# Kernel tuning notes

Measured on AMD Instinct MI355X. Metric: run time of the kernel, lower is better.

The kernel has to match this reference:

```python
import jax, jax.numpy as jnp
import numpy as np

N, M, K, D = 65536, 131072, 8, 64
TAU = 0.3
EPS = 1e-6

def setup_inputs() -> dict:
    key = jax.random.key(0)
    ks = jax.random.split(key, 16)
    s = 0.05
    return {
        "f_pts": jax.random.normal(ks[0], (N, D), jnp.float32),
        "pts": jax.random.uniform(ks[1], (N, 3), jnp.float32) * 10.0,
        "z_latent": jax.random.normal(ks[2], (M, D), jnp.float32) * 0.1,
        "centers": jax.random.uniform(ks[3], (M, 3), jnp.float32) * 10.0,
        "cand_idx": jax.random.randint(ks[4], (N, K), 0, M),
        "sim_w1": jax.random.normal(ks[5], (2 * D + 3, 64), jnp.float32) * s,
        "sim_b1": jnp.zeros((64,), jnp.float32),
        "sim_w2": jax.random.normal(ks[6], (64, 1), jnp.float32) * s,
        "sim_b2": jnp.zeros((1,), jnp.float32),
        "gate_w1": jax.random.normal(ks[7], (2 * D, D), jnp.float32) * s,
        "gate_b1": jnp.zeros((D,), jnp.float32),
        "gate_w2": jax.random.normal(ks[8], (D, 1), jnp.float32) * s,
        "gate_b2": jnp.zeros((1,), jnp.float32),
        "W_ih": jax.random.normal(ks[9], (3 * D, D), jnp.float32) * s,
        "W_hh": jax.random.normal(ks[10], (3 * D, D), jnp.float32) * s,
        "b_ih": jnp.zeros((3 * D,), jnp.float32),
        "b_hh": jnp.zeros((3 * D,), jnp.float32),
    }

def _forward(f_pts, pts, z_latent, centers, sim_w1, sim_b1, sim_w2, sim_b2,
             gate_w1, gate_b1, gate_w2, gate_b2, W_ih, W_hh, b_ih, b_hh, cand_idx):
    n, k = cand_idx.shape
    m, d = z_latent.shape
    # --- gather voxel latents / centers for each (point, candidate) pair ---
    z_c = z_latent[cand_idx]                         # (N,K,D)
    delta = pts[:, None, :] - centers[cand_idx]      # (N,K,3)
    f_b = jnp.broadcast_to(f_pts[:, None, :], (n, k, d))
    # --- similarity MLP ---
    x = jnp.concatenate([f_b, z_c, delta], axis=-1)  # (N,K,2D+3)
    h = jax.nn.relu(x @ sim_w1 + sim_b1)
    sim = (h @ sim_w2 + sim_b2)[..., 0]              # (N,K)
    # --- low-temperature top-K routing weights over candidates ---
    w = jax.nn.softmax(sim / TAU, axis=-1)           # (N,K)
    # --- scatter weighted point features to voxels ---
    flat_idx = cand_idx.reshape(-1)                  # (N*K,)
    contrib = (w[..., None] * f_pts[:, None, :]).reshape(-1, d)
    msg = jax.ops.segment_sum(contrib, flat_idx, num_segments=m)     # (M,D)
    wsum = jax.ops.segment_sum(w.reshape(-1), flat_idx, num_segments=m)
    msg = msg / (wsum[:, None] + EPS)                # normalized voxel message
    # --- per-voxel gate ---
    g_in = jnp.concatenate([z_latent, msg], axis=-1)
    gate = jax.nn.sigmoid(jax.nn.relu(g_in @ gate_w1 + gate_b1) @ gate_w2 + gate_b2)  # (M,1)
    # --- GRUCell (torch layout: rows ordered r,z,n) ---
    gi = msg @ W_ih.T + b_ih
    gh = z_latent @ W_hh.T + b_hh
    i_r, i_z, i_n = jnp.split(gi, 3, axis=-1)
    h_r, h_z, h_n = jnp.split(gh, 3, axis=-1)
    r = jax.nn.sigmoid(i_r + h_r)
    zg = jax.nn.sigmoid(i_z + h_z)
    nn_ = jnp.tanh(i_n + r * h_n)
    h_new = (1.0 - zg) * nn_ + zg * z_latent
    # gated latent update
    return z_latent + gate * (h_new - z_latent)

def reference(f_pts, pts, z_latent, centers, cand_idx, sim_w1, sim_b1, sim_w2, sim_b2,
              gate_w1, gate_b1, gate_w2, gate_b2, W_ih, W_hh, b_ih, b_hh):
    return _forward(f_pts, pts, z_latent, centers, sim_w1, sim_b1, sim_w2, sim_b2,
                    gate_w1, gate_b1, gate_w2, gate_b2, W_ih, W_hh, b_ih, b_hh, cand_idx)
```

## Files before the change

kernel.cpp:

```cpp
#include <hip/hip_runtime.h>
#include <hip/hip_fp16.h>
#include <math.h>


typedef short bf16x8 __attribute__((ext_vector_type(8)));
typedef unsigned short u16x8 __attribute__((ext_vector_type(8)));
typedef float f32x4 __attribute__((ext_vector_type(4)));
#define MFMA __builtin_amdgcn_mfma_f32_16x16x32_bf16
#define CAP 32

__device__ __forceinline__ short f2bf(float f) {
  unsigned u = __float_as_uint(f);
  unsigned r = (u + 0x7FFFu + ((u >> 16) & 1u)) >> 16;
  return (short)r;
}

__device__ __forceinline__ float bf2f(unsigned short h) {
  return __uint_as_float(((unsigned)h) << 16);
}

__device__ __forceinline__ float sigm(float x) { return 1.0f / (1.0f + __expf(-x)); }

__global__ __launch_bounds__(256) void prep_kernel(
    const float* __restrict__ z, const float* __restrict__ f,
    const float* __restrict__ pts, const float* __restrict__ centers,
    const float* __restrict__ sim_w1, const float* __restrict__ sim_b1,
    const float* __restrict__ gate_w1, const float* __restrict__ W_ih,
    const float* __restrict__ W_hh,
    unsigned short* __restrict__ zbf, unsigned short* __restrict__ fbf,
    unsigned short* __restrict__ HBp, unsigned short* __restrict__ ZC,
    short* __restrict__ GF, short* __restrict__ WihF, short* __restrict__ WhhF,
    int* __restrict__ cursor, int M)
{
  long tid = (long)blockIdx.x * 256 + threadIdx.x;
  long nthr = (long)gridDim.x * 256;

  for (long i = tid; i < M; i += nthr) cursor[i] = 0;

  long nz = (long)M * 64;
  for (long i = tid * 8; i < nz; i += nthr * 8) {
    float4 a = *(const float4*)&z[i];
    float4 b4 = *(const float4*)&z[i + 4];
    u16x8 o;
    o[0] = (unsigned short)f2bf(a.x);  o[1] = (unsigned short)f2bf(a.y);
    o[2] = (unsigned short)f2bf(a.z);  o[3] = (unsigned short)f2bf(a.w);
    o[4] = (unsigned short)f2bf(b4.x); o[5] = (unsigned short)f2bf(b4.y);
    o[6] = (unsigned short)f2bf(b4.z); o[7] = (unsigned short)f2bf(b4.w);
    *(u16x8*)&zbf[i] = o;
  }

  if (blockIdx.x >= 1024 && blockIdx.x < 1040) {
    int fb = (blockIdx.x - 1024) * 4 + (threadIdx.x >> 6);
    int lane = threadIdx.x & 63, lr = lane & 15, lg = lane >> 4;
    bf16x8 o;
    if (fb < 16) {
      int ct = fb >> 2, kt = fb & 3;
#pragma unroll
      for (int e = 0; e < 8; ++e)
        o[e] = f2bf(gate_w1[(kt * 32 + lg * 8 + e) * 64 + ct * 16 + lr]);
      *(bf16x8*)&GF[fb * 512 + lane * 8] = o;
    } else if (fb < 40) {
      int q = fb - 16, g = q >> 3, ct = (q >> 1) & 3, k2 = q & 1;
      int row = g * 64 + ct * 16 + lr;
#pragma unroll
      for (int e = 0; e < 8; ++e)
        o[e] = f2bf(W_ih[row * 64 + k2 * 32 + lg * 8 + e]);
      *(bf16x8*)&WihF[q * 512 + lane * 8] = o;
    } else {
      int q = fb - 40, g = q >> 3, ct = (q >> 1) & 3, k2 = q & 1;
      int row = g * 64 + ct * 16 + lr;
#pragma unroll
      for (int e = 0; e < 8; ++e)
        o[e] = f2bf(W_hh[row * 64 + k2 * 32 + lg * 8 + e]);
      *(bf16x8*)&WhhF[q * 512 + lane * 8] = o;
    }
  }

  int g = blockIdx.x * 4 + (threadIdx.x >> 6);
  int lane = threadIdx.x & 63;
  int lr = lane & 15, lg = lane >> 4;

  if (g < 4096) {
    int n0 = g * 16;
    bf16x8 bw[12];
#pragma unroll
    for (int ct = 0; ct < 4; ++ct) {
#pragma unroll
      for (int kt = 0; kt < 2; ++kt) {
        bf16x8 bb;
#pragma unroll
        for (int e = 0; e < 8; ++e)
          bb[e] = f2bf(sim_w1[(kt * 32 + lg * 8 + e) * 64 + ct * 16 + lr]);
        bw[ct * 3 + kt] = bb;
      }
      bf16x8 bb = {0,0,0,0,0,0,0,0};
#pragma unroll
      for (int e = 0; e < 8; ++e) {
        int kk = lg * 8 + e;
        if (kk < 3) bb[e] = f2bf(sim_w1[(128 + kk) * 64 + ct * 16 + lr]);
      }
      bw[ct * 3 + 2] = bb;
    }

    bf16x8 a[3];
#pragma unroll
    for (int kt = 0; kt < 2; ++kt) {
      const float* src = &f[(long)(n0 + lr) * 64 + kt * 32 + lg * 8];
      float4 v0 = *(const float4*)src;
      float4 v1 = *(const float4*)(src + 4);
      bf16x8 t;
      t[0] = f2bf(v0.x); t[1] = f2bf(v0.y); t[2] = f2bf(v0.z); t[3] = f2bf(v0.w);
      t[4] = f2bf(v1.x); t[5] = f2bf(v1.y); t[6] = f2bf(v1.z); t[7] = f2bf(v1.w);
      a[kt] = t;
    }
    {
      bf16x8 t = {0,0,0,0,0,0,0,0};
      if (lg == 0) {
        t[0] = f2bf(pts[(n0 + lr) * 3 + 0]);
        t[1] = f2bf(pts[(n0 + lr) * 3 + 1]);
        t[2] = f2bf(pts[(n0 + lr) * 3 + 2]);
      }
      a[2] = t;
    }
    *(bf16x8*)&fbf[(long)(n0 + lr) * 64 + lg * 8] = a[0];
    *(bf16x8*)&fbf[(long)(n0 + lr) * 64 + 32 + lg * 8] = a[1];

    f32x4 acc[4] = {{0,0,0,0},{0,0,0,0},{0,0,0,0},{0,0,0,0}};
#pragma unroll
    for (int ct = 0; ct < 4; ++ct)
#pragma unroll
      for (int kt = 0; kt < 3; ++kt)
        acc[ct] = MFMA(a[kt], bw[ct * 3 + kt], acc[ct], 0, 0, 0);

#pragma unroll
    for (int ct = 0; ct < 4; ++ct) {
      float b1 = sim_b1[ct * 16 + lr];
#pragma unroll
      for (int e = 0; e < 4; ++e)
        HBp[(long)(n0 + lg * 4 + e) * 64 + ct * 16 + lr] =
            (unsigned short)f2bf(acc[ct][e] + b1);
    }
  } else if (g < 12288) {
    int r0 = (g - 4096) * 16;
    bf16x8 bw[12];
#pragma unroll
    for (int ct = 0; ct < 4; ++ct) {
#pragma unroll
      for (int kt = 0; kt < 2; ++kt) {
        bf16x8 bb;
#pragma unroll
        for (int e = 0; e < 8; ++e)
          bb[e] = f2bf(sim_w1[(64 + kt * 32 + lg * 8 + e) * 64 + ct * 16 + lr]);
        bw[ct * 3 + kt] = bb;
      }
      bf16x8 bb = {0,0,0,0,0,0,0,0};
#pragma unroll
      for (int e = 0; e < 8; ++e) {
        int kk = lg * 8 + e;
        if (kk < 3) bb[e] = f2bf(sim_w1[(128 + kk) * 64 + ct * 16 + lr]);
      }
      bw[ct * 3 + 2] = bb;
    }

    bf16x8 a[3];
#pragma unroll
    for (int kt = 0; kt < 2; ++kt) {
      const float* src = &z[(long)(r0 + lr) * 64 + kt * 32 + lg * 8];
      float4 v0 = *(const float4*)src;
      float4 v1 = *(const float4*)(src + 4);
      bf16x8 t;
      t[0] = f2bf(v0.x); t[1] = f2bf(v0.y); t[2] = f2bf(v0.z); t[3] = f2bf(v0.w);
      t[4] = f2bf(v1.x); t[5] = f2bf(v1.y); t[6] = f2bf(v1.z); t[7] = f2bf(v1.w);
      a[kt] = t;
    }
    {
      bf16x8 t = {0,0,0,0,0,0,0,0};
      if (lg == 0) {
        t[0] = f2bf(-centers[(r0 + lr) * 3 + 0]);
        t[1] = f2bf(-centers[(r0 + lr) * 3 + 1]);
        t[2] = f2bf(-centers[(r0 + lr) * 3 + 2]);
      }
      a[2] = t;
    }

    f32x4 acc[4] = {{0,0,0,0},{0,0,0,0},{0,0,0,0},{0,0,0,0}};
#pragma unroll
    for (int ct = 0; ct < 4; ++ct)
#pragma unroll
      for (int kt = 0; kt < 3; ++kt)
        acc[ct] = MFMA(a[kt], bw[ct * 3 + kt], acc[ct], 0, 0, 0);

#pragma unroll
    for (int ct = 0; ct < 4; ++ct)
#pragma unroll
      for (int e = 0; e < 4; ++e)
        ZC[(long)(r0 + lg * 4 + e) * 64 + ct * 16 + lr] =
            (unsigned short)f2bf(acc[ct][e]);
  }
}

__global__ __launch_bounds__(256) void pair_kernel(
    const unsigned short* __restrict__ HBp, const unsigned short* __restrict__ ZC,
    const int* __restrict__ cand_idx, const float* __restrict__ sim_w2,
    int* __restrict__ cursor, unsigned* __restrict__ rec)
{
  int n = (blockIdx.x * 256 + threadIdx.x) >> 6;
  int lane = threadIdx.x & 63;

  int ci = cand_idx[n * 8 + (lane & 7)];
  int c0 = __builtin_amdgcn_readlane(ci, 0);
  int c1 = __builtin_amdgcn_readlane(ci, 1);
  int c2 = __builtin_amdgcn_readlane(ci, 2);
  int c3 = __builtin_amdgcn_readlane(ci, 3);
  int c4 = __builtin_amdgcn_readlane(ci, 4);
  int c5 = __builtin_amdgcn_readlane(ci, 5);
  int c6 = __builtin_amdgcn_readlane(ci, 6);
  int c7 = __builtin_amdgcn_readlane(ci, 7);

  float hbv = bf2f(HBp[(long)n * 64 + lane]);
  float w2 = sim_w2[lane];
  float p0 = fmaxf(hbv + bf2f(ZC[(long)c0 * 64 + lane]), 0.f) * w2;
  float p1 = fmaxf(hbv + bf2f(ZC[(long)c1 * 64 + lane]), 0.f) * w2;
  float p2 = fmaxf(hbv + bf2f(ZC[(long)c2 * 64 + lane]), 0.f) * w2;
  float p3 = fmaxf(hbv + bf2f(ZC[(long)c3 * 64 + lane]), 0.f) * w2;
  float p4 = fmaxf(hbv + bf2f(ZC[(long)c4 * 64 + lane]), 0.f) * w2;
  float p5 = fmaxf(hbv + bf2f(ZC[(long)c5 * 64 + lane]), 0.f) * w2;
  float p6 = fmaxf(hbv + bf2f(ZC[(long)c6 * 64 + lane]), 0.f) * w2;
  float p7 = fmaxf(hbv + bf2f(ZC[(long)c7 * 64 + lane]), 0.f) * w2;

#pragma unroll
  for (int m = 1; m <= 32; m <<= 1) {
    p0 += __shfl_xor(p0, m, 64);
    p1 += __shfl_xor(p1, m, 64);
    p2 += __shfl_xor(p2, m, 64);
    p3 += __shfl_xor(p3, m, 64);
    p4 += __shfl_xor(p4, m, 64);
    p5 += __shfl_xor(p5, m, 64);
    p6 += __shfl_xor(p6, m, 64);
    p7 += __shfl_xor(p7, m, 64);
  }

  float mx = fmaxf(fmaxf(fmaxf(p0, p1), fmaxf(p2, p3)),
                   fmaxf(fmaxf(p4, p5), fmaxf(p6, p7)));
  float e0 = __expf((p0 - mx) * (1.0f / 0.3f));
  float e1 = __expf((p1 - mx) * (1.0f / 0.3f));
  float e2 = __expf((p2 - mx) * (1.0f / 0.3f));
  float e3 = __expf((p3 - mx) * (1.0f / 0.3f));
  float e4 = __expf((p4 - mx) * (1.0f / 0.3f));
  float e5 = __expf((p5 - mx) * (1.0f / 0.3f));
  float e6 = __expf((p6 - mx) * (1.0f / 0.3f));
  float e7 = __expf((p7 - mx) * (1.0f / 0.3f));
  float inv = 1.0f / (e0 + e1 + e2 + e3 + e4 + e5 + e6 + e7);

  if (lane < 8) {
    float wsel = lane == 0 ? e0 : lane == 1 ? e1 : lane == 2 ? e2 :
                 lane == 3 ? e3 : lane == 4 ? e4 : lane == 5 ? e5 :
                 lane == 6 ? e6 : e7;
    wsel *= inv;
    int slot = atomicAdd(&cursor[ci], 1);
    if (slot < CAP) {
      unsigned short wh = __half_as_ushort(__float2half(wsel));
      rec[(long)ci * CAP + slot] = ((unsigned)n << 16) | (unsigned)wh;
    }
  }
}

__global__ __launch_bounds__(256) void gather_kernel(
    const unsigned* __restrict__ rec, const int* __restrict__ cursor,
    const unsigned short* __restrict__ fbf, unsigned short* __restrict__ msg_bf,
    int mvox)
{
  int tid = blockIdx.x * 256 + threadIdx.x;
  int row = tid >> 2, seg = tid & 3;
  if (row >= mvox) return;

  int cnt = cursor[row];
  cnt = cnt < CAP ? cnt : CAP;
  const unsigned* rp = &rec[(long)row * CAP];

  float acc[16];
#pragma unroll
  for (int j = 0; j < 16; ++j) acc[j] = 0.f;
  float ws = 0.f;

  for (int i0 = 0; i0 < cnt; i0 += 4) {
    uint4 r4 = *(const uint4*)&rp[i0];
    unsigned rr0 = r4.x, rr1 = r4.y, rr2 = r4.z, rr3 = r4.w;
#pragma unroll
    for (int j = 0; j < 4; ++j) {
      unsigned r = j == 0 ? rr0 : j == 1 ? rr1 : j == 2 ? rr2 : rr3;
      if (i0 + j < cnt) {
        float w = __half2float(__ushort_as_half((unsigned short)(r & 0xffffu)));
        int nn = r >> 16;
        ws += w;
        const u16x8* fp = (const u16x8*)&fbf[(long)nn * 64 + seg * 16];
        u16x8 f0 = fp[0], f1 = fp[1];
#pragma unroll
        for (int k = 0; k < 8; ++k) {
          acc[k]     = fmaf(w, bf2f(f0[k]), acc[k]);
          acc[8 + k] = fmaf(w, bf2f(f1[k]), acc[8 + k]);
        }
      }
    }
  }
  float inv = 1.0f / (ws + 1e-6f);
  u16x8 o0, o1;
#pragma unroll
  for (int j = 0; j < 8; ++j) {
    o0[j] = (unsigned short)f2bf(acc[j] * inv);
    o1[j] = (unsigned short)f2bf(acc[8 + j] * inv);
  }
  *(u16x8*)&msg_bf[(long)row * 64 + seg * 16] = o0;
  *(u16x8*)&msg_bf[(long)row * 64 + seg * 16 + 8] = o1;
}

__global__ __launch_bounds__(512)
__attribute__((amdgpu_waves_per_eu(2)))
void stage2(
    const unsigned short* __restrict__ zbf,
    const short* __restrict__ GF, const short* __restrict__ WihF,
    const short* __restrict__ WhhF,
    const float* __restrict__ gate_b1, const float* __restrict__ gate_w2,
    const float* __restrict__ gate_b2,
    const float* __restrict__ b_ih, const float* __restrict__ b_hh,
    const unsigned short* __restrict__ msg_bf,
    float* __restrict__ out)
{
  __shared__ float gb1s[64], gw2s[64], bihs[192], bhhs[192];
  __shared__ float gb2s;

  int t = threadIdx.x;
  if (t < 64) { gb1s[t] = gate_b1[t]; gw2s[t] = gate_w2[t]; }
  if (t < 192) { bihs[t] = b_ih[t]; bhhs[t] = b_hh[t]; }
  if (t == 0) gb2s = gate_b2[0];
  __syncthreads();

  int wid = t >> 6, lane = t & 63;
  int lr = lane & 15, lg = lane >> 4;

  int rowbase = blockIdx.x * 128 + wid * 16;
  long abase = (long)(rowbase + lr) * 64;
  bf16x8 a0 = *(const bf16x8*)&zbf[abase + lg * 8];
  bf16x8 a1 = *(const bf16x8*)&zbf[abase + 32 + lg * 8];
  bf16x8 a2 = *(const bf16x8*)&msg_bf[abase + lg * 8];
  bf16x8 a3 = *(const bf16x8*)&msg_bf[abase + 32 + lg * 8];

  f32x4 usum = {0.f, 0.f, 0.f, 0.f};
#pragma unroll 1
  for (int ct = 0; ct < 4; ++ct) {
    f32x4 au = {0, 0, 0, 0};
    au = MFMA(a0, *(const bf16x8*)&GF[(ct * 4 + 0) * 512 + lane * 8], au, 0, 0, 0);
    au = MFMA(a1, *(const bf16x8*)&GF[(ct * 4 + 1) * 512 + lane * 8], au, 0, 0, 0);
    au = MFMA(a2, *(const bf16x8*)&GF[(ct * 4 + 2) * 512 + lane * 8], au, 0, 0, 0);
    au = MFMA(a3, *(const bf16x8*)&GF[(ct * 4 + 3) * 512 + lane * 8], au, 0, 0, 0);
    int c = ct * 16 + lr;
#pragma unroll
    for (int e = 0; e < 4; ++e)
      usum[e] += fmaxf(au[e] + gb1s[c], 0.0f) * gw2s[c];
  }
#pragma unroll
  for (int m = 1; m <= 8; m <<= 1)
#pragma unroll
    for (int e = 0; e < 4; ++e) {
      float v = usum[e];
      usum[e] = v + __shfl_xor(v, m, 64);
    }
  float gate[4];
#pragma unroll
  for (int e = 0; e < 4; ++e) gate[e] = sigm(usum[e] + gb2s);

#pragma unroll 1
  for (int ct = 0; ct < 4; ++ct) {
    f32x4 air = {0,0,0,0}, aiz = {0,0,0,0}, ain = {0,0,0,0};
    f32x4 ahr = {0,0,0,0}, ahz = {0,0,0,0}, ahn = {0,0,0,0};
#pragma unroll
    for (int k2 = 0; k2 < 2; ++k2) {
      bf16x8 amg = k2 ? a3 : a2;
      bf16x8 az_ = k2 ? a1 : a0;
      int base = ct * 2 + k2;
      air = MFMA(amg, *(const bf16x8*)&WihF[(      base) * 512 + lane * 8], air, 0, 0, 0);
      aiz = MFMA(amg, *(const bf16x8*)&WihF[( 8 +  base) * 512 + lane * 8], aiz, 0, 0, 0);
      ain = MFMA(amg, *(const bf16x8*)&WihF[(16 +  base) * 512 + lane * 8], ain, 0, 0, 0);
      ahr = MFMA(az_, *(const bf16x8*)&WhhF[(      base) * 512 + lane * 8], ahr, 0, 0, 0);
      ahz = MFMA(az_, *(const bf16x8*)&WhhF[( 8 +  base) * 512 + lane * 8], ahz, 0, 0, 0);
      ahn = MFMA(az_, *(const bf16x8*)&WhhF[(16 +  base) * 512 + lane * 8], ahn, 0, 0, 0);
    }
    int c = ct * 16 + lr;
#pragma unroll
    for (int e = 0; e < 4; ++e) {
      float zv = bf2f(zbf[(long)(rowbase + lg * 4 + e) * 64 + c]);
      float rr = sigm(air[e] + bihs[c] + ahr[e] + bhhs[c]);
      float zg = sigm(aiz[e] + bihs[64 + c] + ahz[e] + bhhs[64 + c]);
      float nn = tanhf(ain[e] + bihs[128 + c] + rr * (ahn[e] + bhhs[128 + c]));
      float hnew = (1.0f - zg) * nn + zg * zv;
      out[(long)(rowbase + lg * 4 + e) * 64 + c] = zv + gate[e] * (hnew - zv);
    }
  }
}

extern "C" void kernel_launch(void* const* d_in, const int* in_sizes, int n_in,
                              void* d_out, int out_size, void* d_ws, size_t ws_size,
                              hipStream_t stream) {
  const float* f_pts   = (const float*)d_in[0];
  const float* pts     = (const float*)d_in[1];
  const float* z_lat   = (const float*)d_in[2];
  const float* centers = (const float*)d_in[3];
  const int*   cand    = (const int*)d_in[4];
  const float* sim_w1  = (const float*)d_in[5];
  const float* sim_b1  = (const float*)d_in[6];
  const float* sim_w2  = (const float*)d_in[7];
  const float* gate_w1 = (const float*)d_in[9];
  const float* gate_b1 = (const float*)d_in[10];
  const float* gate_w2 = (const float*)d_in[11];
  const float* gate_b2 = (const float*)d_in[12];
  const float* W_ih    = (const float*)d_in[13];
  const float* W_hh    = (const float*)d_in[14];
  const float* b_ih    = (const float*)d_in[15];
  const float* b_hh    = (const float*)d_in[16];

  int N = in_sizes[0] / 64;
  int M = in_sizes[2] / 64;

  int* cursor = (int*)d_ws;
  unsigned* rec = (unsigned*)(cursor + M);
  unsigned short* msg_bf = (unsigned short*)rec;
  unsigned short* zbf = (unsigned short*)(rec + (size_t)M * CAP);
  unsigned short* fbf = zbf + (size_t)M * 64;
  unsigned short* HBp = fbf + (size_t)N * 64;
  unsigned short* ZC = HBp + (size_t)N * 64;
  short* GF = (short*)(ZC + (size_t)M * 64);
  short* WihF = GF + 16 * 512;
  short* WhhF = WihF + 24 * 512;

  prep_kernel<<<3072, 256, 0, stream>>>(z_lat, f_pts, pts, centers,
                                        sim_w1, sim_b1, gate_w1, W_ih, W_hh,
                                        zbf, fbf, HBp, ZC, GF, WihF, WhhF,
                                        cursor, M);

  pair_kernel<<<N / 4, 256, 0, stream>>>(HBp, ZC, cand, sim_w2, cursor, rec);

  gather_kernel<<<(M * 4) / 256, 256, 0, stream>>>(rec, cursor, fbf, msg_bf, M);

  stage2<<<M / 128, 512, 0, stream>>>(zbf, GF, WihF, WhhF,
                                      gate_b1, gate_w2, gate_b2, b_ih, b_hh,
                                      msg_bf, (float*)d_out);
}
```

Measured before the change: 119.3 us.

## Precompute weight fragments once, fuse z bf16 conversion, vectorize pair scoring

Adds a small prep0 kernel that converts all weight matrices to bf16 MFMA fragment layout once and zeroes the cursor array, so each prep wave loads ready fragments instead of reconverting sim_w1 from fp32. The separate z-to-bf16 loop is removed; the z fragments already loaded for the ZC projection are written out as zbf. The pair kernel is restructured so each lane handles one candidate and an 8-element channel slice with vector loads, shrinking the shuffle reductions and exp count. It adds one more kernel launch and relies on the new fragment buffers being laid out correctly in the workspace.

Result: faster. 102.4 us (-14.2%).

```diff
diff --git a/kernel.cpp b/kernel.cpp
--- a/kernel.cpp
+++ b/kernel.cpp
@@ -21,61 +21,76 @@
 
 __device__ __forceinline__ float sigm(float x) { return 1.0f / (1.0f + __expf(-x)); }
 
+__global__ __launch_bounds__(256) void prep0_kernel(
+    const float* __restrict__ sim_w1, const float* __restrict__ gate_w1,
+    const float* __restrict__ W_ih, const float* __restrict__ W_hh,
+    short* __restrict__ bfF, short* __restrict__ bfZC,
+    short* __restrict__ GF, short* __restrict__ WihF, short* __restrict__ WhhF,
+    int* __restrict__ cursor, int M)
+{
+  int tid = blockIdx.x * 256 + threadIdx.x;
+  int n4 = M >> 2;
+  int stride = gridDim.x * 256;
+  int4* cp = (int4*)cursor;
+  for (int j = tid; j < n4; j += stride) cp[j] = make_int4(0, 0, 0, 0);
+
+  int w = blockIdx.x * 4 + (threadIdx.x >> 6);
+  int lane = threadIdx.x & 63, lr = lane & 15, lg = lane >> 4;
+  bf16x8 o;
+
+  if (w < 12) {
+    int ct = w / 3, kt = w % 3;
+#pragma unroll
+    for (int e = 0; e < 8; ++e) {
+      int k = kt * 32 + lg * 8 + e;
+      float v = 0.0f;
+      if (kt < 2) v = sim_w1[k * 64 + ct * 16 + lr];
+      else if ((k - 64) < 3) v = sim_w1[(128 + (k - 64)) * 64 + ct * 16 + lr];
+      o[e] = f2bf(v);
+    }
+    *(bf16x8*)&bfF[w * 512 + lane * 8] = o;
+  } else if (w < 24) {
+    int q = w - 12, ct = q / 3, kt = q % 3;
+#pragma unroll
+    for (int e = 0; e < 8; ++e) {
+      int k = kt * 32 + lg * 8 + e;
+      float v = 0.0f;
+      if (kt < 2) v = sim_w1[(64 + k) * 64 + ct * 16 + lr];
+      else if ((k - 64) < 3) v = sim_w1[(128 + (k - 64)) * 64 + ct * 16 + lr];
+      o[e] = f2bf(v);
+    }
+    *(bf16x8*)&bfZC[q * 512 + lane * 8] = o;
+  } else if (w < 40) {
+    int q = w - 24, ct = q >> 2, kt = q & 3;
+#pragma unroll
+    for (int e = 0; e < 8; ++e)
+      o[e] = f2bf(gate_w1[(kt * 32 + lg * 8 + e) * 64 + ct * 16 + lr]);
+    *(bf16x8*)&GF[q * 512 + lane * 8] = o;
+  } else if (w < 64) {
+    int q = w - 40, g = q >> 3, ct = (q >> 1) & 3, k2 = q & 1;
+    int row = g * 64 + ct * 16 + lr;
+#pragma unroll
+    for (int e = 0; e < 8; ++e)
+      o[e] = f2bf(W_ih[row * 64 + k2 * 32 + lg * 8 + e]);
+    *(bf16x8*)&WihF[q * 512 + lane * 8] = o;
+  } else if (w < 88) {
+    int q = w - 64, g = q >> 3, ct = (q >> 1) & 3, k2 = q & 1;
+    int row = g * 64 + ct * 16 + lr;
+#pragma unroll
+    for (int e = 0; e < 8; ++e)
+      o[e] = f2bf(W_hh[row * 64 + k2 * 32 + lg * 8 + e]);
+    *(bf16x8*)&WhhF[q * 512 + lane * 8] = o;
+  }
+}
+
 __global__ __launch_bounds__(256) void prep_kernel(
     const float* __restrict__ z, const float* __restrict__ f,
     const float* __restrict__ pts, const float* __restrict__ centers,
-    const float* __restrict__ sim_w1, const float* __restrict__ sim_b1,
-    const float* __restrict__ gate_w1, const float* __restrict__ W_ih,
-    const float* __restrict__ W_hh,
+    const float* __restrict__ sim_b1,
+    const short* __restrict__ bfF, const short* __restrict__ bfZC,
     unsigned short* __restrict__ zbf, unsigned short* __restrict__ fbf,
-    unsigned short* __restrict__ HBp, unsigned short* __restrict__ ZC,
-    short* __restrict__ GF, short* __restrict__ WihF, short* __restrict__ WhhF,
-    int* __restrict__ cursor, int M)
+    unsigned short* __restrict__ HBp, unsigned short* __restrict__ ZC)
 {
-  long tid = (long)blockIdx.x * 256 + threadIdx.x;
-  long nthr = (long)gridDim.x * 256;
-
-  for (long i = tid; i < M; i += nthr) cursor[i] = 0;
-
-  long nz = (long)M * 64;
-  for (long i = tid * 8; i < nz; i += nthr * 8) {
-    float4 a = *(const float4*)&z[i];
-    float4 b4 = *(const float4*)&z[i + 4];
-    u16x8 o;
-    o[0] = (unsigned short)f2bf(a.x);  o[1] = (unsigned short)f2bf(a.y);
-    o[2] = (unsigned short)f2bf(a.z);  o[3] = (unsigned short)f2bf(a.w);
-    o[4] = (unsigned short)f2bf(b4.x); o[5] = (unsigned short)f2bf(b4.y);
-    o[6] = (unsigned short)f2bf(b4.z); o[7] = (unsigned short)f2bf(b4.w);
-    *(u16x8*)&zbf[i] = o;
-  }
-
-  if (blockIdx.x >= 1024 && blockIdx.x < 1040) {
-    int fb = (blockIdx.x - 1024) * 4 + (threadIdx.x >> 6);
-    int lane = threadIdx.x & 63, lr = lane & 15, lg = lane >> 4;
-    bf16x8 o;
-    if (fb < 16) {
-      int ct = fb >> 2, kt = fb & 3;
-#pragma unroll
-      for (int e = 0; e < 8; ++e)
-        o[e] = f2bf(gate_w1[(kt * 32 + lg * 8 + e) * 64 + ct * 16 + lr]);
-      *(bf16x8*)&GF[fb * 512 + lane * 8] = o;
-    } else if (fb < 40) {
-      int q = fb - 16, g = q >> 3, ct = (q >> 1) & 3, k2 = q & 1;
-      int row = g * 64 + ct * 16 + lr;
-#pragma unroll
-      for (int e = 0; e < 8; ++e)
-        o[e] = f2bf(W_ih[row * 64 + k2 * 32 + lg * 8 + e]);
-      *(bf16x8*)&WihF[q * 512 + lane * 8] = o;
-    } else {
-      int q = fb - 40, g = q >> 3, ct = (q >> 1) & 3, k2 = q & 1;
-      int row = g * 64 + ct * 16 + lr;
-#pragma unroll
-      for (int e = 0; e < 8; ++e)
-        o[e] = f2bf(W_hh[row * 64 + k2 * 32 + lg * 8 + e]);
-      *(bf16x8*)&WhhF[q * 512 + lane * 8] = o;
-    }
-  }
-
   int g = blockIdx.x * 4 + (threadIdx.x >> 6);
   int lane = threadIdx.x & 63;
   int lr = lane & 15, lg = lane >> 4;
@@ -84,23 +99,7 @@
     int n0 = g * 16;
     bf16x8 bw[12];
 #pragma unroll
-    for (int ct = 0; ct < 4; ++ct) {
-#pragma unroll
-      for (int kt = 0; kt < 2; ++kt) {
-        bf16x8 bb;
-#pragma unroll
-        for (int e = 0; e < 8; ++e)
-          bb[e] = f2bf(sim_w1[(kt * 32 + lg * 8 + e) * 64 + ct * 16 + lr]);
-        bw[ct * 3 + kt] = bb;
-      }
-      bf16x8 bb = {0,0,0,0,0,0,0,0};
-#pragma unroll
-      for (int e = 0; e < 8; ++e) {
-        int kk = lg * 8 + e;
-        if (kk < 3) bb[e] = f2bf(sim_w1[(128 + kk) * 64 + ct * 16 + lr]);
-      }
-      bw[ct * 3 + 2] = bb;
-    }
+    for (int i = 0; i < 12; ++i) bw[i] = *(const bf16x8*)&bfF[i * 512 + lane * 8];
 
     bf16x8 a[3];
 #pragma unroll
@@ -144,23 +143,7 @@
     int r0 = (g - 4096) * 16;
     bf16x8 bw[12];
 #pragma unroll
-    for (int ct = 0; ct < 4; ++ct) {
-#pragma unroll
-      for (int kt = 0; kt < 2; ++kt) {
-        bf16x8 bb;
-#pragma unroll
-        for (int e = 0; e < 8; ++e)
-          bb[e] = f2bf(sim_w1[(64 + kt * 32 + lg * 8 + e) * 64 + ct * 16 + lr]);
-        bw[ct * 3 + kt] = bb;
-      }
-      bf16x8 bb = {0,0,0,0,0,0,0,0};
-#pragma unroll
-      for (int e = 0; e < 8; ++e) {
-        int kk = lg * 8 + e;
-        if (kk < 3) bb[e] = f2bf(sim_w1[(128 + kk) * 64 + ct * 16 + lr]);
-      }
-      bw[ct * 3 + 2] = bb;
-    }
+    for (int i = 0; i < 12; ++i) bw[i] = *(const bf16x8*)&bfZC[i * 512 + lane * 8];
 
     bf16x8 a[3];
 #pragma unroll
@@ -182,6 +165,8 @@
       }
       a[2] = t;
     }
+    *(bf16x8*)&zbf[(long)(r0 + lr) * 64 + lg * 8] = a[0];
+    *(bf16x8*)&zbf[(long)(r0 + lr) * 64 + 32 + lg * 8] = a[1];
 
     f32x4 acc[4] = {{0,0,0,0},{0,0,0,0},{0,0,0,0},{0,0,0,0}};
 #pragma unroll
@@ -206,60 +191,47 @@
 {
   int n = (blockIdx.x * 256 + threadIdx.x) >> 6;
   int lane = threadIdx.x & 63;
-
-  int ci = cand_idx[n * 8 + (lane & 7)];
-  int c0 = __builtin_amdgcn_readlane(ci, 0);
-  int c1 = __builtin_amdgcn_readlane(ci, 1);
-  int c2 = __builtin_amdgcn_readlane(ci, 2);
-  int c3 = __builtin_amdgcn_readlane(ci, 3);
-  int c4 = __builtin_amdgcn_readlane(ci, 4);
-  int c5 = __builtin_amdgcn_readlane(ci, 5);
-  int c6 = __builtin_amdgcn_readlane(ci, 6);
-  int c7 = __builtin_amdgcn_readlane(ci, 7);
-
-  float hbv = bf2f(HBp[(long)n * 64 + lane]);
-  float w2 = sim_w2[lane];
-  float p0 = fmaxf(hbv + bf2f(ZC[(long)c0 * 64 + lane]), 0.f) * w2;
-  float p1 = fmaxf(hbv + bf2f(ZC[(long)c1 * 64 + lane]), 0.f) * w2;
-  float p2 = fmaxf(hbv + bf2f(ZC[(long)c2 * 64 + lane]), 0.f) * w2;
-  float p3 = fmaxf(hbv + bf2f(ZC[(long)c3 * 64 + lane]), 0.f) * w2;
-  float p4 = fmaxf(hbv + bf2f(ZC[(long)c4 * 64 + lane]), 0.f) * w2;
-  float p5 = fmaxf(hbv + bf2f(ZC[(long)c5 * 64 + lane]), 0.f) * w2;
-  float p6 = fmaxf(hbv + bf2f(ZC[(long)c6 * 64 + lane]), 0.f) * w2;
-  float p7 = fmaxf(hbv + bf2f(ZC[(long)c7 * 64 + lane]), 0.f) * w2;
-
-#pragma unroll
-  for (int m = 1; m <= 32; m <<= 1) {
-    p0 += __shfl_xor(p0, m, 64);
-    p1 += __shfl_xor(p1, m, 64);
-    p2 += __shfl_xor(p2, m, 64);
-    p3 += __shfl_xor(p3, m, 64);
-    p4 += __shfl_xor(p4, m, 64);
-    p5 += __shfl_xor(p5, m, 64);
-    p6 += __shfl_xor(p6, m, 64);
-    p7 += __shfl_xor(p7, m, 64);
-  }
-
-  float mx = fmaxf(fmaxf(fmaxf(p0, p1), fmaxf(p2, p3)),
-                   fmaxf(fmaxf(p4, p5), fmaxf(p6, p7)));
-  float e0 = __expf((p0 - mx) * (1.0f / 0.3f));
-  float e1 = __expf((p1 - mx) * (1.0f / 0.3f));
-  float e2 = __expf((p2 - mx) * (1.0f / 0.3f));
-  float e3 = __expf((p3 - mx) * (1.0f / 0.3f));
-  float e4 = __expf((p4 - mx) * (1.0f / 0.3f));
-  float e5 = __expf((p5 - mx) * (1.0f / 0.3f));
-  float e6 = __expf((p6 - mx) * (1.0f / 0.3f));
-  float e7 = __expf((p7 - mx) * (1.0f / 0.3f));
-  float inv = 1.0f / (e0 + e1 + e2 + e3 + e4 + e5 + e6 + e7);
+  int k = lane & 7, cg = lane >> 3;
+
+  int ci = cand_idx[n * 8 + k];
+
+  uint4 zc4 = *(const uint4*)&ZC[(long)ci * 64 + cg * 8];
+  uint4 hb4 = *(const uint4*)&HBp[(long)n * 64 + cg * 8];
+  float4 w2a = *(const float4*)&sim_w2[cg * 8];
+  float4 w2b = *(const float4*)&sim_w2[cg * 8 + 4];
+
+  float s = 0.f;
+  {
+    unsigned zd[4] = {zc4.x, zc4.y, zc4.z, zc4.w};
+    unsigned hd[4] = {hb4.x, hb4.y, hb4.z, hb4.w};
+    float w2v[8] = {w2a.x, w2a.y, w2a.z, w2a.w, w2b.x, w2b.y, w2b.z, w2b.w};
+#pragma unroll
+    for (int d = 0; d < 4; ++d) {
+      float zlo = __uint_as_float(zd[d] << 16);
+      float zhi = __uint_as_float(zd[d] & 0xffff0000u);
+      float hlo = __uint_as_float(hd[d] << 16);
+      float hhi = __uint_as_float(hd[d] & 0xffff0000u);
+      s = fmaf(fmaxf(hlo + zlo, 0.f), w2v[2 * d], s);
+      s = fmaf(fmaxf(hhi + zhi, 0.f), w2v[2 * d + 1], s);
+    }
+  }
+
+#pragma unroll
+  for (int m = 8; m <= 32; m <<= 1) s += __shfl_xor(s, m, 64);
+
+  float mx = s;
+#pragma unroll
+  for (int m = 1; m <= 4; m <<= 1) mx = fmaxf(mx, __shfl_xor(mx, m, 64));
+  float e = __expf((s - mx) * (1.0f / 0.3f));
+  float ss = e;
+#pragma unroll
+  for (int m = 1; m <= 4; m <<= 1) ss += __shfl_xor(ss, m, 64);
+  float w = e / ss;
 
   if (lane < 8) {
-    float wsel = lane == 0 ? e0 : lane == 1 ? e1 : lane == 2 ? e2 :
-                 lane == 3 ? e3 : lane == 4 ? e4 : lane == 5 ? e5 :
-                 lane == 6 ? e6 : e7;
-    wsel *= inv;
     int slot = atomicAdd(&cursor[ci], 1);
     if (slot < CAP) {
-      unsigned short wh = __half_as_ushort(__float2half(wsel));
+      unsigned short wh = __half_as_ushort(__float2half(w));
       rec[(long)ci * CAP + slot] = ((unsigned)n << 16) | (unsigned)wh;
     }
   }
@@ -296,9 +268,9 @@
         const u16x8* fp = (const u16x8*)&fbf[(long)nn * 64 + seg * 16];
         u16x8 f0 = fp[0], f1 = fp[1];
 #pragma unroll
-        for (int k = 0; k < 8; ++k) {
-          acc[k]     = fmaf(w, bf2f(f0[k]), acc[k]);
-          acc[8 + k] = fmaf(w, bf2f(f1[k]), acc[8 + k]);
+        for (int kk = 0; kk < 8; ++kk) {
+          acc[kk]     = fmaf(w, bf2f(f0[kk]), acc[kk]);
+          acc[8 + kk] = fmaf(w, bf2f(f1[kk]), acc[8 + kk]);
         }
       }
     }
@@ -428,14 +400,17 @@
   unsigned short* fbf = zbf + (size_t)M * 64;
   unsigned short* HBp = fbf + (size_t)N * 64;
   unsigned short* ZC = HBp + (size_t)N * 64;
-  short* GF = (short*)(ZC + (size_t)M * 64);
+  short* bfF = (short*)(ZC + (size_t)M * 64);
+  short* bfZC = bfF + 12 * 512;
+  short* GF = bfZC + 12 * 512;
   short* WihF = GF + 16 * 512;
   short* WhhF = WihF + 24 * 512;
 
-  prep_kernel<<<3072, 256, 0, stream>>>(z_lat, f_pts, pts, centers,
-                                        sim_w1, sim_b1, gate_w1, W_ih, W_hh,
-                                        zbf, fbf, HBp, ZC, GF, WihF, WhhF,
-                                        cursor, M);
+  prep0_kernel<<<32, 256, 0, stream>>>(sim_w1, gate_w1, W_ih, W_hh,
+                                       bfF, bfZC, GF, WihF, WhhF, cursor, M);
+
+  prep_kernel<<<3072, 256, 0, stream>>>(z_lat, f_pts, pts, centers, sim_b1,
+                                        bfF, bfZC, zbf, fbf, HBp, ZC);
 
   pair_kernel<<<N / 4, 256, 0, stream>>>(HBp, ZC, cand, sim_w2, cursor, rec);
 
```
